# Kernel tuning notes

Hardware: AMD Instinct MI355X
Metric: run time of the kernel (lower is better)

## Reference

```python
import jax, jax.numpy as jnp
import numpy as np

B, T, DM, H, R = 2, 2048, 1024, 16, 8
HD = DM // H
LORA_SCALE = 16.0 / R  # alpha / r


def setup_inputs() -> dict:
    key = jax.random.key(0)
    ks = jax.random.split(key, 8)
    return {
        "hidden_states": jax.random.normal(ks[0], (B, T, DM), jnp.float32),
        "attention_mask": jnp.zeros((B, 1, 1, T), jnp.float32),
        "Wq": jax.random.normal(ks[1], (DM, DM), jnp.float32) * 0.02,
        "bq": jnp.zeros((DM,), jnp.float32),
        "Aq": jax.random.normal(ks[2], (R, DM), jnp.float32) * 0.02,
        "Bq": jax.random.normal(ks[3], (DM, R), jnp.float32) * 0.02,
        "Wk": jax.random.normal(ks[4], (DM, DM), jnp.float32) * 0.02,
        "bk": jnp.zeros((DM,), jnp.float32),
        "Wv": jax.random.normal(ks[5], (DM, DM), jnp.float32) * 0.02,
        "bv": jnp.zeros((DM,), jnp.float32),
        "Av": jax.random.normal(ks[6], (R, DM), jnp.float32) * 0.02,
        "Bv": jax.random.normal(ks[7], (DM, R), jnp.float32) * 0.02,
    }


def _lora_linear(x, W, b, A, Bmat):
    # y = x W^T + b + scale * (x A^T) B^T   (lora_dropout = 0 in eval)
    return x @ W.T + b + LORA_SCALE * ((x @ A.T) @ Bmat.T)


def _heads(x):
    # [b, t, (h d)] -> [b, h, t, d]
    b, t, _ = x.shape
    return x.reshape(b, t, H, HD).transpose(0, 2, 1, 3)


def reference(hidden_states, attention_mask, Wq, bq, Aq, Bq, Wk, bk, Wv, bv, Av, Bv):
    q = _heads(_lora_linear(hidden_states, Wq, bq, Aq, Bq))
    k = _heads(hidden_states @ Wk.T + bk)
    v = _heads(_lora_linear(hidden_states, Wv, bv, Av, Bv))

    scores = jnp.einsum("bhtd,bhsd->bhts", q, k) * (HD ** -0.5)
    causal = jnp.triu(jnp.ones((T, T), dtype=bool), k=1)[None, None]
    scores = jnp.where(causal, jnp.float32(-jnp.inf), scores)
    scores = scores + attention_mask
    probs = jax.nn.softmax(scores, axis=-1)  # dropout p=0 (eval)
    attn = jnp.einsum("bhts,bhsd->bhtd", probs, v)
    # [b, h, t, d] -> [b, t, h*d]
    return attn.transpose(0, 2, 1, 3).reshape(B, T, DM)
```

## Files before the change

### kernel.cpp

```cpp
#include <hip/hip_runtime.h>
#include <hip/hip_bf16.h>

#define BB 2
#define TT 2048
#define DMM 1024
#define HH 16
#define HDD 64

typedef __attribute__((ext_vector_type(8))) short bf16x8;
typedef __attribute__((ext_vector_type(4))) short short4v;
typedef __attribute__((ext_vector_type(4))) float f32x4;

static __device__ __forceinline__ short f2bf(float f) {
    __hip_bfloat16 h = __float2bfloat16(f);
    return *reinterpret_cast<short*>(&h);
}

static __device__ __forceinline__ float ex2(float x) {
    return __builtin_amdgcn_exp2f(x);
}

static __device__ __forceinline__ void gl_lds16(const void* g, void* l) {
    __builtin_amdgcn_global_load_lds(
        (const __attribute__((address_space(1))) void*)g,
        (__attribute__((address_space(3))) void*)l, 16, 0, 0);
}

__global__ void cvt_hidden(const float* __restrict__ x, short* __restrict__ y) {
    int i = blockIdx.x * 256 + threadIdx.x;
    float4 v = reinterpret_cast<const float4*>(x)[i];
    short4v o;
    o[0] = f2bf(v.x); o[1] = f2bf(v.y); o[2] = f2bf(v.z); o[3] = f2bf(v.w);
    reinterpret_cast<short4v*>(y)[i] = o;
}

__global__ void prep_w(const float* __restrict__ Wq, const float* __restrict__ Aq, const float* __restrict__ Bq,
                       const float* __restrict__ Wk,
                       const float* __restrict__ Wv, const float* __restrict__ Av, const float* __restrict__ Bv,
                       short* __restrict__ Wqe, short* __restrict__ Wke, short* __restrict__ Wve) {
    const int mode = blockIdx.y;
    const float* W = (mode == 0) ? Wq : (mode == 1) ? Wk : Wv;
    const float* A = (mode == 0) ? Aq : Av;
    const float* Bm = (mode == 0) ? Bq : Bv;
    short* outp = (mode == 0) ? Wqe : (mode == 1) ? Wke : Wve;
    int idx = blockIdx.x * 256 + threadIdx.x;
    int n = idx >> 10, k = idx & 1023;
    float v = W[idx];
    if (mode != 1) {
        float s = 0.f;
#pragma unroll
        for (int r = 0; r < 8; ++r) s += Bm[n * 8 + r] * A[r * 1024 + k];
        v += 2.0f * s;
    }
    outp[idx] = f2bf(v);
}

__global__ __launch_bounds__(256) void proj_fused(
        const short* __restrict__ Xbf,
        const short* __restrict__ Wqe, const short* __restrict__ Wke, const short* __restrict__ Wve,
        const float* __restrict__ bq, const float* __restrict__ bk, const float* __restrict__ bv,
        short* __restrict__ Qb, short* __restrict__ Kb, short* __restrict__ Vtb) {
    __shared__ __align__(16) char XS[4096];
    __shared__ __align__(16) char WS[3][8192];

    const int tid = threadIdx.x;
    const int wave = tid >> 6, lane = tid & 63;
    const int l15 = lane & 15, l4 = lane >> 4;
    const int bx = blockIdx.x, by = blockIdx.y;
    const int wx = 2 * (bx & 3) + (by & 1);
    const int wy = (bx >> 2) * 32 + (by >> 1);
    const int m0 = wy * 64, n0 = wx * 128;
    const int wm = (wave >> 1) * 32, wn = (wave & 1) * 64;

    const int srow_x = wave * 16 + (lane >> 2);
    const int srow_w = wave * 32 + (lane >> 2);
    const int srcc = ((lane & 3) ^ ((lane >> 3) & 3)) * 8;

    f32x4 aq[4][2] = {}, ak[4][2] = {}, av[2][4] = {};

    for (int k0 = 0; k0 < 1024; k0 += 32) {
        __syncthreads();
        gl_lds16(Xbf + (m0 + srow_x) * 1024 + k0 + srcc, XS + wave * 1024);
        gl_lds16(Wqe + (n0 + srow_w) * 1024 + k0 + srcc, WS[0] + wave * 2048);
        gl_lds16(Wqe + (n0 + srow_w + 16) * 1024 + k0 + srcc, WS[0] + wave * 2048 + 1024);
        gl_lds16(Wke + (n0 + srow_w) * 1024 + k0 + srcc, WS[1] + wave * 2048);
        gl_lds16(Wke + (n0 + srow_w + 16) * 1024 + k0 + srcc, WS[1] + wave * 2048 + 1024);
        gl_lds16(Wve + (n0 + srow_w) * 1024 + k0 + srcc, WS[2] + wave * 2048);
        gl_lds16(Wve + (n0 + srow_w + 16) * 1024 + k0 + srcc, WS[2] + wave * 2048 + 1024);
        __syncthreads();

        bf16x8 xf[2];
#pragma unroll
        for (int x = 0; x < 2; ++x) {
            int r = wm + x * 16 + l15;
            xf[x] = *reinterpret_cast<const bf16x8*>(XS + r * 64 + ((l4 ^ ((r >> 1) & 3)) << 4));
        }
        {
            bf16x8 wf[4];
#pragma unroll
            for (int w = 0; w < 4; ++w) {
                int r = wn + w * 16 + l15;
                wf[w] = *reinterpret_cast<const bf16x8*>(WS[0] + r * 64 + ((l4 ^ ((r >> 1) & 3)) << 4));
            }
#pragma unroll
            for (int w = 0; w < 4; ++w)
#pragma unroll
                for (int x = 0; x < 2; ++x)
                    aq[w][x] = __builtin_amdgcn_mfma_f32_16x16x32_bf16(wf[w], xf[x], aq[w][x], 0, 0, 0);
        }
        {
            bf16x8 wf[4];
#pragma unroll
            for (int w = 0; w < 4; ++w) {
                int r = wn + w * 16 + l15;
                wf[w] = *reinterpret_cast<const bf16x8*>(WS[1] + r * 64 + ((l4 ^ ((r >> 1) & 3)) << 4));
            }
#pragma unroll
            for (int w = 0; w < 4; ++w)
#pragma unroll
                for (int x = 0; x < 2; ++x)
                    ak[w][x] = __builtin_amdgcn_mfma_f32_16x16x32_bf16(wf[w], xf[x], ak[w][x], 0, 0, 0);
        }
        {
            bf16x8 wf[4];
#pragma unroll
            for (int w = 0; w < 4; ++w) {
                int r = wn + w * 16 + l15;
                wf[w] = *reinterpret_cast<const bf16x8*>(WS[2] + r * 64 + ((l4 ^ ((r >> 1) & 3)) << 4));
            }
#pragma unroll
            for (int x = 0; x < 2; ++x)
#pragma unroll
                for (int w = 0; w < 4; ++w)
                    av[x][w] = __builtin_amdgcn_mfma_f32_16x16x32_bf16(xf[x], wf[w], av[x][w], 0, 0, 0);
        }
    }

#pragma unroll
    for (int w = 0; w < 4; ++w) {
        int gnb = n0 + wn + w * 16 + l4 * 4;
        int hh = gnb >> 6, d = gnb & 63;
        float4 bv4 = *reinterpret_cast<const float4*>(bq + gnb);
#pragma unroll
        for (int x = 0; x < 2; ++x) {
            int gm = m0 + wm + x * 16 + l15;
            int bb = gm >> 11, t = gm & 2047;
            short4v o;
            o[0] = f2bf((aq[w][x][0] + bv4.x) * 0.18033688f);
            o[1] = f2bf((aq[w][x][1] + bv4.y) * 0.18033688f);
            o[2] = f2bf((aq[w][x][2] + bv4.z) * 0.18033688f);
            o[3] = f2bf((aq[w][x][3] + bv4.w) * 0.18033688f);
            *reinterpret_cast<short4v*>(Qb + ((bb * 16 + hh) * 2048 + t) * 64 + d) = o;
        }
    }
#pragma unroll
    for (int w = 0; w < 4; ++w) {
        int gnb = n0 + wn + w * 16 + l4 * 4;
        int hh = gnb >> 6, d = gnb & 63;
        float4 bv4 = *reinterpret_cast<const float4*>(bk + gnb);
#pragma unroll
        for (int x = 0; x < 2; ++x) {
            int gm = m0 + wm + x * 16 + l15;
            int bb = gm >> 11, t = gm & 2047;
            short4v o;
            o[0] = f2bf(ak[w][x][0] + bv4.x);
            o[1] = f2bf(ak[w][x][1] + bv4.y);
            o[2] = f2bf(ak[w][x][2] + bv4.z);
            o[3] = f2bf(ak[w][x][3] + bv4.w);
            *reinterpret_cast<short4v*>(Kb + ((bb * 16 + hh) * 2048 + t) * 64 + d) = o;
        }
    }
#pragma unroll
    for (int x = 0; x < 2; ++x) {
        int gmb = m0 + wm + x * 16 + l4 * 4;
        int bb = gmb >> 11, t = gmb & 2047;
#pragma unroll
        for (int w = 0; w < 4; ++w) {
            int gn = n0 + wn + w * 16 + l15;
            int hh = gn >> 6, d = gn & 63;
            int tx = ((gn >> 3) & 1) << 2;
            float bvs = bv[gn];
            short4v o;
            o[0] = f2bf(av[x][w][0] + bvs);
            o[1] = f2bf(av[x][w][1] + bvs);
            o[2] = f2bf(av[x][w][2] + bvs);
            o[3] = f2bf(av[x][w][3] + bvs);
            *reinterpret_cast<short4v*>(Vtb + ((bb * 16 + hh) * 64 + d) * 2048 + (t ^ tx)) = o;
        }
    }
}


#define STAGE(BUF, T) do {                                                           \
    const int _kv = (T) << 5;                                                        \
    gl_lds16(Kp + (_kv + krow) * 64 + kswz, MEM + (BUF) * 4096 + wv * 1024);         \
    gl_lds16(Vp + lane * 2048 + _kv + wv * 8, MEM + 16384 + (BUF) * 4096 + wv * 1024);\
} while (0)

#define SLICEJOB(QF0, QF1, OO, M, L, QBASE) do {                                     \
    f32x4 ss = {};                                                                   \
    ss = __builtin_amdgcn_mfma_f32_16x16x32_bf16(kf0, QF0, ss, 0, 0, 0);             \
    ss = __builtin_amdgcn_mfma_f32_16x16x32_bf16(kf1, QF1, ss, 0, 0, 0);             \
    float pr[4];                                                                     \
    if (kvs + 15 > (QBASE)) {                                                        \
        _Pragma("unroll")                                                            \
        for (int r = 0; r < 4; ++r) {                                                \
            float v = ss[r] + mv[r];                                                 \
            if (kvs + l4*4 + r > (QBASE) + l15) v = -1e30f;                          \
            pr[r] = v;                                                               \
        }                                                                            \
    } else {                                                                         \
        _Pragma("unroll")                                                            \
        for (int r = 0; r < 4; ++r) pr[r] = ss[r] + mv[r];                           \
    }                                                                                \
    float tl = fmaxf(fmaxf(pr[0], pr[1]), fmaxf(pr[2], pr[3]));                      \
    if (!__all(tl - (M) <= 11.5415603f)) {                                           \
        float tm = tl;                                                               \
        tm = fmaxf(tm, __shfl_xor(tm, 16));                                          \
        tm = fmaxf(tm, __shfl_xor(tm, 32));                                          \
        float mn = fmaxf((M), tm);                                                   \
        float al = ex2((M) - mn);                                                    \
        M = mn; L *= al;                                                             \
        _Pragma("unroll")                                                            \
        for (int dt = 0; dt < 4; ++dt)                                               \
            _Pragma("unroll")                                                        \
            for (int r = 0; r < 4; ++r) OO[dt][r] *= al;                             \
    }                                                                                \
    _Pragma("unroll")                                                                \
    for (int r = 0; r < 4; ++r) pr[r] = ex2(pr[r] - (M));                            \
    L += (pr[0] + pr[1]) + (pr[2] + pr[3]);                                          \
    short4v pa;                                                                      \
    _Pragma("unroll")                                                                \
    for (int r = 0; r < 4; ++r) pa[r] = f2bf(pr[r]);                                 \
    _Pragma("unroll")                                                                \
    for (int dt = 0; dt < 4; ++dt)                                                   \
        OO[dt] = __builtin_amdgcn_mfma_f32_16x16x16bf16_1k(vf[dt], pa, OO[dt], 0, 0, 0); \
} while (0)

#define AITER(BUF, T) do {                                                           \
    if ((T) + 2 < NT) {                                                              \
        STAGE((((BUF) + 2) & 3), (T) + 2);                                           \
        asm volatile("s_waitcnt vmcnt(4)" ::: "memory");                             \
    } else if ((T) + 1 < NT) {                                                       \
        asm volatile("s_waitcnt vmcnt(2)" ::: "memory");                             \
    } else {                                                                         \
        asm volatile("s_waitcnt vmcnt(0)" ::: "memory");                             \
    }                                                                                \
    asm volatile("s_barrier" ::: "memory");                                          \
    if ((T) < nkA) {                                                                 \
        const char* Kcur = MEM + (BUF) * 4096;                                       \
        const char* Vcur = MEM + 16384 + (BUF) * 4096;                               \
        bf16x8 kf0 = *reinterpret_cast<const bf16x8*>(Kcur + kb0);                   \
        bf16x8 kf1 = *reinterpret_cast<const bf16x8*>(Kcur + (kb0 ^ 64));            \
        short4v vf[4];                                                               \
        _Pragma("unroll")                                                            \
        for (int dt = 0; dt < 4; ++dt)                                               \
            vf[dt] = *reinterpret_cast<const short4v*>(Vcur + vb0 + dt * 256);       \
        const int kvs = ((T) << 5) + 16 * s;                                         \
        float4 mv = *reinterpret_cast<const float4*>(mlds + kvs + l4 * 4);           \
        SLICEJOB(qfA0, qfA1, OA, MA, LA, qbaseA);                                    \
        if ((T) < nkB) SLICEJOB(qfB0, qfB1, OB, MB, LB, qbaseB);                     \
    }                                                                                \
} while (0)

__global__ __launch_bounds__(256, 4) void attn(
        const short* __restrict__ Qb, const short* __restrict__ Kb,
        const short* __restrict__ Vt, const float* __restrict__ amask,
        float* __restrict__ outp) {
    __shared__ __align__(16) char MEM[40960];

    const int tid = threadIdx.x, wv = tid >> 6, lane = tid & 63;
    const int l15 = lane & 15, l4 = lane >> 4;
    const int xcd = blockIdx.x & 7;
    const int k   = blockIdx.x >> 3;
    const int j   = ((k >> 5) << 3) | ((k & 3) << 1) | ((k >> 4) & 1);
    const int bh  = xcd * 4 + ((k >> 2) & 3);
    const int p  = wv & 1;
    const int s  = wv >> 1;
    const int i  = 2 * j + p;
    const int b = bh >> 4, h = bh & 15;

    const short* Qp = Qb + bh * TT * HDD;
    const short* Kp = Kb + bh * TT * HDD;
    const short* Vp = Vt + bh * HDD * TT;
    const float* mp = amask + b * TT;
    float* mlds = (float*)(MEM + 32768);

    const int qbaseA = (127 - i) << 4;
    const int qbaseB = i << 4;
    const int nkA = ((qbaseA + 15 - 16 * s) >> 5) + 1;
    const int nkB = ((qbaseB + 15 - 16 * s) >> 5) + 1;
    const int NT = ((127 - 2 * j) * 16 + 47) >> 5;

    const int krow = wv * 8 + (lane >> 3);
    const int kswz = ((lane & 7) ^ (lane >> 3)) * 8;

    const int kb0 = (16 * s + l15) * 128 + ((l4 ^ (l15 & 7)) << 4);
    const int vb0 = (2 * s + (l4 >> 1)) * 1024 + l15 * 16 + (((l4 & 1) ^ (l15 >> 3)) << 3);

    {
        int mi8 = tid * 8;
        float4 a = *reinterpret_cast<const float4*>(mp + mi8);
        float4 c = *reinterpret_cast<const float4*>(mp + mi8 + 4);
        a.x *= 1.44269504f; a.y *= 1.44269504f; a.z *= 1.44269504f; a.w *= 1.44269504f;
        c.x *= 1.44269504f; c.y *= 1.44269504f; c.z *= 1.44269504f; c.w *= 1.44269504f;
        *reinterpret_cast<float4*>(mlds + mi8) = a;
        *reinterpret_cast<float4*>(mlds + mi8 + 4) = c;
    }

    bf16x8 qfA0 = *reinterpret_cast<const bf16x8*>(Qp + (qbaseA + l15) * 64 + l4 * 8);
    bf16x8 qfA1 = *reinterpret_cast<const bf16x8*>(Qp + (qbaseA + l15) * 64 + 32 + l4 * 8);
    bf16x8 qfB0 = *reinterpret_cast<const bf16x8*>(Qp + (qbaseB + l15) * 64 + l4 * 8);
    bf16x8 qfB1 = *reinterpret_cast<const bf16x8*>(Qp + (qbaseB + l15) * 64 + 32 + l4 * 8);

    f32x4 OA[4] = {}, OB[4] = {};
    float MA = -1e30f, LA = 0.f, MB = -1e30f, LB = 0.f;

    STAGE(0, 0);
    STAGE(1, 1);
    asm volatile("s_waitcnt lgkmcnt(0)" ::: "memory");

    int t = 0;
    for (; t + 4 <= NT; t += 4) {
        AITER(0, t);
        AITER(1, t + 1);
        AITER(2, t + 2);
        AITER(3, t + 3);
    }
    for (; t < NT; ++t) AITER((t & 3), t);

    asm volatile("s_barrier" ::: "memory");

    LA += __shfl_xor(LA, 16); LA += __shfl_xor(LA, 32);
    LB += __shfl_xor(LB, 16); LB += __shfl_xor(LB, 32);

    float* mg = (float*)MEM + p * 2560 + lane * 40;
    if (s) {
#pragma unroll
        for (int dt = 0; dt < 4; ++dt) *reinterpret_cast<f32x4*>(mg + dt * 4) = OA[dt];
        mg[16] = MA; mg[17] = LA;
#pragma unroll
        for (int dt = 0; dt < 4; ++dt) *reinterpret_cast<f32x4*>(mg + 20 + dt * 4) = OB[dt];
        mg[36] = MB; mg[37] = LB;
    }
    __syncthreads();
    if (!s) {
        {
            float m1 = mg[16], l1 = mg[17];
            float ms = fmaxf(MA, m1);
            float e0 = ex2(MA - ms), e1 = ex2(m1 - ms);
            float inv = 1.0f / (LA * e0 + l1 * e1);
            int tA = qbaseA + l15;
#pragma unroll
            for (int dt = 0; dt < 4; ++dt) {
                f32x4 o1 = *reinterpret_cast<const f32x4*>(mg + dt * 4);
                float4 o;
                o.x = (OA[dt][0] * e0 + o1[0] * e1) * inv;
                o.y = (OA[dt][1] * e0 + o1[1] * e1) * inv;
                o.z = (OA[dt][2] * e0 + o1[2] * e1) * inv;
                o.w = (OA[dt][3] * e0 + o1[3] * e1) * inv;
                *reinterpret_cast<float4*>(outp + (b * 2048 + tA) * 1024 + h * 64 + dt * 16 + l4 * 4) = o;
            }
        }
        {
            float m1 = mg[36], l1 = mg[37];
            float ms = fmaxf(MB, m1);
            float e0 = ex2(MB - ms), e1 = ex2(m1 - ms);
            float inv = 1.0f / (LB * e0 + l1 * e1);
            int tB = qbaseB + l15;
#pragma unroll
            for (int dt = 0; dt < 4; ++dt) {
                f32x4 o1 = *reinterpret_cast<const f32x4*>(mg + 20 + dt * 4);
                float4 o;
                o.x = (OB[dt][0] * e0 + o1[0] * e1) * inv;
                o.y = (OB[dt][1] * e0 + o1[1] * e1) * inv;
                o.z = (OB[dt][2] * e0 + o1[2] * e1) * inv;
                o.w = (OB[dt][3] * e0 + o1[3] * e1) * inv;
                *reinterpret_cast<float4*>(outp + (b * 2048 + tB) * 1024 + h * 64 + dt * 16 + l4 * 4) = o;
            }
        }
    }
}

extern "C" void kernel_launch(void* const* d_in, const int* in_sizes, int n_in,
                              void* d_out, int out_size, void* d_ws, size_t ws_size,
                              hipStream_t stream) {
    const float* hidden = (const float*)d_in[0];
    const float* amask  = (const float*)d_in[1];
    const float* Wq = (const float*)d_in[2];
    const float* bq = (const float*)d_in[3];
    const float* Aq = (const float*)d_in[4];
    const float* Bq = (const float*)d_in[5];
    const float* Wk = (const float*)d_in[6];
    const float* bk = (const float*)d_in[7];
    const float* Wv = (const float*)d_in[8];
    const float* bv = (const float*)d_in[9];
    const float* Av = (const float*)d_in[10];
    const float* Bv = (const float*)d_in[11];
    float* outp = (float*)d_out;

    char* ws = (char*)d_ws;
    short* Xbf = (short*)(ws);
    short* Wqe = (short*)(ws + (8 << 20));
    short* Wke = (short*)(ws + (10 << 20));
    short* Wve = (short*)(ws + (12 << 20));
    short* Qb  = (short*)(ws + (14 << 20));
    short* Kb  = (short*)(ws + (22 << 20));
    short* Vtb = (short*)(ws + (30 << 20));

    cvt_hidden<<<4096, 256, 0, stream>>>(hidden, Xbf);
    prep_w<<<dim3(4096, 3), 256, 0, stream>>>(Wq, Aq, Bq, Wk, Wv, Av, Bv, Wqe, Wke, Wve);
    proj_fused<<<dim3(8, 64), 256, 0, stream>>>(Xbf, Wqe, Wke, Wve, bq, bk, bv, Qb, Kb, Vtb);
    attn<<<1024, 256, 0, stream>>>(Qb, Kb, Vtb, amask, outp);
}
```

Measured before the change: 102.9 us.

## Prefetch attention-mask slices into registers instead of staging in LDS

Removes the LDS-staged copy of the scaled attention mask. Each iteration now loads its mask float4 straight from global memory two tiles ahead, rotating through register slots, and folds the log2e scaling in at use time. The vmcnt waits are raised to account for the extra outstanding load. Freeing 8 KB of LDS allows launch bounds to go from 4 to 5 blocks per CU, trading more registers and extra global loads for higher occupancy.

```diff
diff --git a/kernel.cpp b/kernel.cpp
--- a/kernel.cpp
+++ b/kernel.cpp
@@ -237,12 +237,13 @@
         OO[dt] = __builtin_amdgcn_mfma_f32_16x16x16bf16_1k(vf[dt], pa, OO[dt], 0, 0, 0); \
 } while (0)
 
-#define AITER(BUF, T) do {                                                           \
+#define AITER(BUF, T, MVC, MVP) do {                                                 \
     if ((T) + 2 < NT) {                                                              \
         STAGE((((BUF) + 2) & 3), (T) + 2);                                           \
-        asm volatile("s_waitcnt vmcnt(4)" ::: "memory");                             \
+        MVP = *reinterpret_cast<const float4*>(mp + (((T) + 2) << 5) + 16 * s + l4 * 4); \
+        asm volatile("s_waitcnt vmcnt(6)" ::: "memory");                             \
     } else if ((T) + 1 < NT) {                                                       \
-        asm volatile("s_waitcnt vmcnt(2)" ::: "memory");                             \
+        asm volatile("s_waitcnt vmcnt(3)" ::: "memory");                             \
     } else {                                                                         \
         asm volatile("s_waitcnt vmcnt(0)" ::: "memory");                             \
     }                                                                                \
@@ -257,17 +258,19 @@
         for (int dt = 0; dt < 4; ++dt)                                               \
             vf[dt] = *reinterpret_cast<const short4v*>(Vcur + vb0 + dt * 256);       \
         const int kvs = ((T) << 5) + 16 * s;                                         \
-        float4 mv = *reinterpret_cast<const float4*>(mlds + kvs + l4 * 4);           \
+        float4 mv;                                                                   \
+        mv.x = MVC.x * 1.44269504f; mv.y = MVC.y * 1.44269504f;                      \
+        mv.z = MVC.z * 1.44269504f; mv.w = MVC.w * 1.44269504f;                      \
         SLICEJOB(qfA0, qfA1, OA, MA, LA, qbaseA);                                    \
         if ((T) < nkB) SLICEJOB(qfB0, qfB1, OB, MB, LB, qbaseB);                     \
     }                                                                                \
 } while (0)
 
-__global__ __launch_bounds__(256, 4) void attn(
+__global__ __launch_bounds__(256, 5) void attn(
         const short* __restrict__ Qb, const short* __restrict__ Kb,
         const short* __restrict__ Vt, const float* __restrict__ amask,
         float* __restrict__ outp) {
-    __shared__ __align__(16) char MEM[40960];
+    __shared__ __align__(16) char MEM[32768];
 
     const int tid = threadIdx.x, wv = tid >> 6, lane = tid & 63;
     const int l15 = lane & 15, l4 = lane >> 4;
@@ -284,7 +287,6 @@
     const short* Kp = Kb + bh * TT * HDD;
     const short* Vp = Vt + bh * HDD * TT;
     const float* mp = amask + b * TT;
-    float* mlds = (float*)(MEM + 32768);
 
     const int qbaseA = (127 - i) << 4;
     const int qbaseB = i << 4;
@@ -298,16 +300,6 @@
     const int kb0 = (16 * s + l15) * 128 + ((l4 ^ (l15 & 7)) << 4);
     const int vb0 = (2 * s + (l4 >> 1)) * 1024 + l15 * 16 + (((l4 & 1) ^ (l15 >> 3)) << 3);
 
-    {
-        int mi8 = tid * 8;
-        float4 a = *reinterpret_cast<const float4*>(mp + mi8);
-        float4 c = *reinterpret_cast<const float4*>(mp + mi8 + 4);
-        a.x *= 1.44269504f; a.y *= 1.44269504f; a.z *= 1.44269504f; a.w *= 1.44269504f;
-        c.x *= 1.44269504f; c.y *= 1.44269504f; c.z *= 1.44269504f; c.w *= 1.44269504f;
-        *reinterpret_cast<float4*>(mlds + mi8) = a;
-        *reinterpret_cast<float4*>(mlds + mi8 + 4) = c;
-    }
-
     bf16x8 qfA0 = *reinterpret_cast<const bf16x8*>(Qp + (qbaseA + l15) * 64 + l4 * 8);
     bf16x8 qfA1 = *reinterpret_cast<const bf16x8*>(Qp + (qbaseA + l15) * 64 + 32 + l4 * 8);
     bf16x8 qfB0 = *reinterpret_cast<const bf16x8*>(Qp + (qbaseB + l15) * 64 + l4 * 8);
@@ -315,19 +307,22 @@
 
     f32x4 OA[4] = {}, OB[4] = {};
     float MA = -1e30f, LA = 0.f, MB = -1e30f, LB = 0.f;
+    float4 mv0 = {0, 0, 0, 0}, mv1 = {0, 0, 0, 0}, mv2 = {0, 0, 0, 0}, mv3 = {0, 0, 0, 0};
 
     STAGE(0, 0);
+    mv0 = *reinterpret_cast<const float4*>(mp + 16 * s + l4 * 4);
     STAGE(1, 1);
-    asm volatile("s_waitcnt lgkmcnt(0)" ::: "memory");
-
-    int t = 0;
-    for (; t + 4 <= NT; t += 4) {
-        AITER(0, t);
-        AITER(1, t + 1);
-        AITER(2, t + 2);
-        AITER(3, t + 3);
-    }
-    for (; t < NT; ++t) AITER((t & 3), t);
+    mv1 = *reinterpret_cast<const float4*>(mp + 32 + 16 * s + l4 * 4);
+
+    for (int t = 0; t < NT; t += 4) {
+        AITER(0, t, mv0, mv2);
+        if (t + 1 >= NT) break;
+        AITER(1, t + 1, mv1, mv3);
+        if (t + 2 >= NT) break;
+        AITER(2, t + 2, mv2, mv0);
+        if (t + 3 >= NT) break;
+        AITER(3, t + 3, mv3, mv1);
+    }
 
     asm volatile("s_barrier" ::: "memory");
 
```

Measured after the change: 189.8 us. +84.6%, slower.
